# Optimization experiments

Measured on AMD Instinct MI355X. Metric: run time of the kernel, lower is better.

The kernel has to match this reference:

```python
import jax, jax.numpy as jnp
import numpy as np

HIDDEN = 1024
NUM_HEADS = 16
HEAD_DIM = HIDDEN // NUM_HEADS  # 64
ROPE_DIM = HEAD_DIM // 2        # 32 (per-axis rotary dim)
EPS = 1e-6


def _make_rope_tables(dim, grid_h, grid_w, theta=10000.0):
    # pt_seq_len == ft_seq_len, so t_h = arange(H), t_w = arange(W)
    freqs = 1.0 / theta ** (np.arange(0, dim, 2, dtype=np.float32)[: dim // 2] / dim)  # [dim//2]
    fh = np.repeat(np.outer(np.arange(grid_h, dtype=np.float32), freqs), 2, axis=-1)  # [H, dim]
    fw = np.repeat(np.outer(np.arange(grid_w, dtype=np.float32), freqs), 2, axis=-1)  # [W, dim]
    fh = np.broadcast_to(fh[:, None, :], (grid_h, grid_w, dim))
    fw = np.broadcast_to(fw[None, :, :], (grid_h, grid_w, dim))
    f2d = np.concatenate([fh, fw], axis=-1).reshape(grid_h * grid_w, 2 * dim)  # [HW, 2*dim]
    return jnp.asarray(np.cos(f2d)), jnp.asarray(np.sin(f2d))


def _rms_norm(x, w, eps=EPS):
    var = jnp.mean(jnp.square(x), axis=-1, keepdims=True)
    return x * jax.lax.rsqrt(var + eps) * w


def _rotate_half(x):
    x1 = x[..., 0::2]
    x2 = x[..., 1::2]
    return jnp.stack([-x2, x1], axis=-1).reshape(x.shape)


def _apply_rope(x, cos, sin):
    # x: [B, H, S, D]; cos/sin: [S, D]
    return x * cos + _rotate_half(x) * sin


def setup_inputs() -> dict:
    key = jax.random.key(0)
    ks = jax.random.split(key, 12)
    B, IMG_H, IMG_W, CND_H, CND_W = 2, 64, 64, 32, 32
    img_len, cnd_len = IMG_H * IMG_W, CND_H * CND_W
    xav = (6.0 / (HIDDEN + HIDDEN)) ** 0.5
    inp = {
        'image_tokens': jax.random.normal(ks[0], (B, img_len, HIDDEN), jnp.float32),
        'condition_tokens': jax.random.normal(ks[1], (B, cnd_len, HIDDEN), jnp.float32),
        'q_norm_w': jnp.ones((HIDDEN,), jnp.float32),
        'kv_norm_w': jnp.ones((HIDDEN,), jnp.float32),
        'q_head_norm_w': jnp.ones((HEAD_DIM,), jnp.float32),
        'k_head_norm_w': jnp.ones((HEAD_DIM,), jnp.float32),
        'q_w': jax.random.uniform(ks[2], (HIDDEN, HIDDEN), jnp.float32, -xav, xav),
        'q_b': jnp.zeros((HIDDEN,), jnp.float32),
        'k_w': jax.random.uniform(ks[3], (HIDDEN, HIDDEN), jnp.float32, -xav, xav),
        'k_b': jnp.zeros((HIDDEN,), jnp.float32),
        'v_w': jax.random.uniform(ks[4], (HIDDEN, HIDDEN), jnp.float32, -xav, xav),
        'v_b': jnp.zeros((HIDDEN,), jnp.float32),
        'o_w': jax.random.uniform(ks[5], (HIDDEN, HIDDEN), jnp.float32, -xav, xav),
        'o_b': jnp.zeros((HIDDEN,), jnp.float32),
        'alpha': jnp.full((1,), 0.5, jnp.float32),  # nonzero so backward exercises the attn path
    }
    ic, isn = _make_rope_tables(ROPE_DIM, IMG_H, IMG_W)
    cc, cs = _make_rope_tables(ROPE_DIM, CND_H, CND_W)
    inp.update(image_cos=ic, image_sin=isn, cond_cos=cc, cond_sin=cs)
    return inp


def reference(image_tokens, condition_tokens, q_norm_w, kv_norm_w, q_head_norm_w,
              k_head_norm_w, q_w, q_b, k_w, k_b, v_w, v_b, o_w, o_b, alpha,
              image_cos, image_sin, cond_cos, cond_sin):
    B, Li, _ = image_tokens.shape
    Lc = condition_tokens.shape[1]
    qn = _rms_norm(image_tokens, q_norm_w)
    kvn = _rms_norm(condition_tokens, kv_norm_w)
    # projections (torch Linear: x @ W.T + b); weights here stored [out, in]
    q = (qn @ q_w.T + q_b).reshape(B, Li, NUM_HEADS, HEAD_DIM).transpose(0, 2, 1, 3)
    k = (kvn @ k_w.T + k_b).reshape(B, Lc, NUM_HEADS, HEAD_DIM).transpose(0, 2, 1, 3)
    v = (kvn @ v_w.T + v_b).reshape(B, Lc, NUM_HEADS, HEAD_DIM).transpose(0, 2, 1, 3)
    q = _rms_norm(q, q_head_norm_w)
    k = _rms_norm(k, k_head_norm_w)
    q = _apply_rope(q, image_cos, image_sin)
    k = _apply_rope(k, cond_cos, cond_sin)
    scale = 1.0 / jnp.sqrt(jnp.asarray(HEAD_DIM, q.dtype))
    scores = jnp.einsum('bhqd,bhkd->bhqk', q, k) * scale
    attn = jax.nn.softmax(scores, axis=-1)
    out = jnp.einsum('bhqk,bhkd->bhqd', attn, v)
    out = out.transpose(0, 2, 1, 3).reshape(B, Li, HIDDEN)
    update = out @ o_w.T + o_b
    return image_tokens + alpha.reshape(1, 1, 1) * update
```

## Files before the change

### kernel.cpp

```cpp
#include <hip/hip_runtime.h>

typedef __bf16 bf16x8 __attribute__((ext_vector_type(8)));
typedef __bf16 bf16x4 __attribute__((ext_vector_type(4)));
typedef float  f32x4  __attribute__((ext_vector_type(4)));
typedef float  f32x16 __attribute__((ext_vector_type(16)));
typedef unsigned u32x2 __attribute__((ext_vector_type(2)));

#define DEVINL __device__ __forceinline__

DEVINL void gload_lds16(const void* g, void* l) {
  __builtin_amdgcn_global_load_lds((const __attribute__((address_space(1))) void*)g,
                                   (__attribute__((address_space(3))) void*)l, 16, 0, 0);
}

DEVINL unsigned pkbf(float a, float b) {
  union { __bf16 h[2]; unsigned u; } c;
  c.h[0] = (__bf16)a; c.h[1] = (__bf16)b;
  return c.u;
}

DEVINL float fast_exp2(float x) {
#if __has_builtin(__builtin_amdgcn_exp2f)
  return __builtin_amdgcn_exp2f(x);
#else
  float r;
  asm volatile("v_exp_f32 %0, %1" : "=v"(r) : "v"(x));
  return r;
#endif
}

DEVINL float2 swap32(float x) {
  u32x2 r = __builtin_amdgcn_permlane32_swap(__float_as_uint(x), __float_as_uint(x), false, false);
  return make_float2(__uint_as_float(r.x), __uint_as_float(r.y));
}

__global__ __launch_bounds__(256) void prep_kernel(
    const float* __restrict__ XA, const float* __restrict__ WA, __bf16* __restrict__ YA,
    const float* __restrict__ XB, const float* __restrict__ WB, __bf16* __restrict__ YB,
    const float* __restrict__ wq, const float* __restrict__ wk,
    const float* __restrict__ wv, const float* __restrict__ wo,
    __bf16* __restrict__ oq, __bf16* __restrict__ ok,
    __bf16* __restrict__ ov, __bf16* __restrict__ oo) {
  int rb = blockIdx.x, tid = threadIdx.x;
  if (rb < 10240) {
    const float* X; const float* W; __bf16* Y; int row;
    if (rb < 8192) { X = XA; W = WA; Y = YA; row = rb; }
    else { X = XB; W = WB; Y = YB; row = rb - 8192; }
    const float4* xr = (const float4*)(X + (size_t)row * 1024);
    float4 v = xr[tid];
    float ss = v.x * v.x + v.y * v.y + v.z * v.z + v.w * v.w;
#pragma unroll
    for (int m = 1; m < 64; m <<= 1) ss += __shfl_xor(ss, m);
    __shared__ float part[4];
    if ((tid & 63) == 0) part[tid >> 6] = ss;
    __syncthreads();
    float tot = part[0] + part[1] + part[2] + part[3];
    float rn = rsqrtf(tot * (1.0f / 1024.0f) + 1e-6f);
    float4 wv4 = ((const float4*)W)[tid];
    bf16x4 y;
    y[0] = (__bf16)(v.x * rn * wv4.x);
    y[1] = (__bf16)(v.y * rn * wv4.y);
    y[2] = (__bf16)(v.z * rn * wv4.z);
    y[3] = (__bf16)(v.w * rn * wv4.w);
    *(bf16x4*)(Y + (size_t)row * 1024 + tid * 4) = y;
  } else {
    int gid = (rb - 10240) * 256 + tid;
    int which = gid >> 17;
    size_t off = (size_t)(gid & 131071) * 8;
    const float* s = (which == 0) ? wq : (which == 1) ? wk : (which == 2) ? wv : wo;
    __bf16* o = (which == 0) ? oq : (which == 1) ? ok : (which == 2) ? ov : oo;
    float4 v0 = *(const float4*)(s + off), v1 = *(const float4*)(s + off + 4);
    bf16x8 y;
    y[0] = (__bf16)v0.x; y[1] = (__bf16)v0.y; y[2] = (__bf16)v0.z; y[3] = (__bf16)v0.w;
    y[4] = (__bf16)v1.x; y[5] = (__bf16)v1.y; y[6] = (__bf16)v1.z; y[7] = (__bf16)v1.w;
    *(bf16x8*)(o + off) = y;
  }
}

__global__ __launch_bounds__(256) void qkv_gemm_kernel(
    const __bf16* __restrict__ qn, const __bf16* __restrict__ kvn,
    const __bf16* __restrict__ wq, const __bf16* __restrict__ wkv,
    const float* __restrict__ qb, const float* __restrict__ kb, const float* __restrict__ vb,
    __bf16* __restrict__ Qt, __bf16* __restrict__ Kt, __bf16* __restrict__ Vt0) {
  __shared__ __attribute__((aligned(16))) __bf16 As[128 * 32];
  __shared__ __attribute__((aligned(16))) __bf16 Bs[128 * 32];
  int id = blockIdx.x;
  const __bf16 *A, *Bw; const float* bias; __bf16* Cout;
  int m0, n0, nloc;
  if (id < 512) {
    A = qn; Bw = wq; m0 = (id & 63) * 128; n0 = (id >> 6) * 128; nloc = n0;
    bias = qb; Cout = Qt;
  } else {
    int i2 = id - 512;
    A = kvn; Bw = wkv; m0 = (i2 & 15) * 128; n0 = (i2 >> 4) * 128;
    if (n0 < 1024) { bias = kb; Cout = Kt; nloc = n0; }
    else { bias = vb; Cout = Vt0; nloc = n0 - 1024; }
  }
  int tid = threadIdx.x, lane = tid & 63, w = tid >> 6, wr = w >> 1, wc = w & 1;
  f32x4 z4 = {0.f, 0.f, 0.f, 0.f};
  f32x4 acc[4][4];
#pragma unroll
  for (int i = 0; i < 4; i++)
#pragma unroll
    for (int j = 0; j < 4; j++) acc[i][j] = z4;

  for (int k0 = 0; k0 < 1024; k0 += 32) {
#pragma unroll
    for (int i = 0; i < 2; i++) {
      int chunk = i * 256 + tid;
      int row = chunk >> 2, cc = chunk & 3;
      gload_lds16(A + (size_t)(m0 + row) * 1024 + k0 + cc * 8, (char*)As + i * 4096 + w * 1024);
      gload_lds16(Bw + (size_t)(n0 + row) * 1024 + k0 + cc * 8, (char*)Bs + i * 4096 + w * 1024);
    }
    __syncthreads();
    bf16x8 af[4], bfr[4];
#pragma unroll
    for (int m = 0; m < 4; m++) {
      int r = wr * 64 + m * 16 + (lane & 15);
      af[m] = *(const bf16x8*)((const char*)As + r * 64 + ((lane >> 4) << 4));
    }
#pragma unroll
    for (int n = 0; n < 4; n++) {
      int r = wc * 64 + n * 16 + (lane & 15);
      bfr[n] = *(const bf16x8*)((const char*)Bs + r * 64 + ((lane >> 4) << 4));
    }
#pragma unroll
    for (int m = 0; m < 4; m++)
#pragma unroll
      for (int n = 0; n < 4; n++)
        acc[m][n] = __builtin_amdgcn_mfma_f32_16x16x32_bf16(af[m], bfr[n], acc[m][n], 0, 0, 0);
    __syncthreads();
  }

#pragma unroll
  for (int m = 0; m < 4; m++)
#pragma unroll
    for (int n = 0; n < 4; n++) {
      int col = nloc + wc * 64 + n * 16 + (lane & 15);
      float bv = bias[col];
#pragma unroll
      for (int r = 0; r < 4; r++) {
        int row = m0 + wr * 64 + m * 16 + ((lane >> 4) << 2) + r;
        size_t idx = ((size_t)row << 10) + col;
        Cout[idx] = (__bf16)(acc[m][n][r] + bv);
      }
    }
}

__global__ __launch_bounds__(256) void gemm_o_kernel(
    const __bf16* __restrict__ A, const __bf16* __restrict__ Bw,
    const float* __restrict__ bias, float* __restrict__ Cout,
    const float* __restrict__ resid, const float* __restrict__ alphap) {
  __shared__ __attribute__((aligned(16))) __bf16 As[128 * 32];
  __shared__ __attribute__((aligned(16))) __bf16 Bs[128 * 32];
  int tid = threadIdx.x, lane = tid & 63, w = tid >> 6, wr = w >> 1, wc = w & 1;
  int m0 = blockIdx.x * 128, n0 = blockIdx.y * 128;
  f32x4 z4 = {0.f, 0.f, 0.f, 0.f};
  f32x4 acc[4][4];
#pragma unroll
  for (int i = 0; i < 4; i++)
#pragma unroll
    for (int j = 0; j < 4; j++) acc[i][j] = z4;

  for (int k0 = 0; k0 < 1024; k0 += 32) {
#pragma unroll
    for (int i = 0; i < 2; i++) {
      int chunk = i * 256 + tid;
      int row = chunk >> 2, cc = chunk & 3;
      gload_lds16(A + (size_t)(m0 + row) * 1024 + k0 + cc * 8, (char*)As + i * 4096 + w * 1024);
      gload_lds16(Bw + (size_t)(n0 + row) * 1024 + k0 + cc * 8, (char*)Bs + i * 4096 + w * 1024);
    }
    __syncthreads();
    bf16x8 af[4], bfr[4];
#pragma unroll
    for (int m = 0; m < 4; m++) {
      int r = wr * 64 + m * 16 + (lane & 15);
      af[m] = *(const bf16x8*)((const char*)As + r * 64 + ((lane >> 4) << 4));
    }
#pragma unroll
    for (int n = 0; n < 4; n++) {
      int r = wc * 64 + n * 16 + (lane & 15);
      bfr[n] = *(const bf16x8*)((const char*)Bs + r * 64 + ((lane >> 4) << 4));
    }
#pragma unroll
    for (int m = 0; m < 4; m++)
#pragma unroll
      for (int n = 0; n < 4; n++)
        acc[m][n] = __builtin_amdgcn_mfma_f32_16x16x32_bf16(af[m], bfr[n], acc[m][n], 0, 0, 0);
    __syncthreads();
  }

  float aval = alphap[0];
#pragma unroll
  for (int m = 0; m < 4; m++)
#pragma unroll
    for (int n = 0; n < 4; n++) {
      int col = n0 + wc * 64 + n * 16 + (lane & 15);
      float bv = bias[col];
#pragma unroll
      for (int r = 0; r < 4; r++) {
        int row = m0 + wr * 64 + m * 16 + ((lane >> 4) << 2) + r;
        size_t idx = ((size_t)row << 10) + col;
        Cout[idx] = resid[idx] + aval * (acc[m][n][r] + bv);
      }
    }
}

__global__ __launch_bounds__(256) void kprep_kernel(
    const __bf16* __restrict__ Kt, const float* __restrict__ KHW,
    const float* __restrict__ CCOS, const float* __restrict__ CSIN,
    __bf16* __restrict__ Kr,
    const __bf16* __restrict__ V, __bf16* __restrict__ Vt) {
  int rb = blockIdx.x, tid = threadIdx.x;
  if (rb < 1024) {
    int inst = rb * 32 + (tid >> 3);
    int sub = tid & 7;
    int token = inst >> 4, h = inst & 15;
    int b = token >> 10, pos = token & 1023;
    const __bf16* xp = Kt + ((size_t)token << 10) + h * 64 + sub * 8;
    bf16x8 xv = *(const bf16x8*)xp;
    float xf[8];
#pragma unroll
    for (int i = 0; i < 8; i++) xf[i] = (float)xv[i];
    float ss = 0.f;
#pragma unroll
    for (int i = 0; i < 8; i++) ss += xf[i] * xf[i];
    ss += __shfl_xor(ss, 1);
    ss += __shfl_xor(ss, 2);
    ss += __shfl_xor(ss, 4);
    float rn = rsqrtf(ss * (1.0f / 64.0f) + 1e-6f);
    const float* hwp = KHW + sub * 8;
    const float* cp = CCOS + ((size_t)pos << 6) + sub * 8;
    const float* sp = CSIN + ((size_t)pos << 6) + sub * 8;
    float xn[8], o[8];
#pragma unroll
    for (int i = 0; i < 8; i++) xn[i] = xf[i] * rn * hwp[i];
#pragma unroll
    for (int i = 0; i < 8; i += 2) {
      o[i] = xn[i] * cp[i] - xn[i + 1] * sp[i];
      o[i + 1] = xn[i + 1] * cp[i + 1] + xn[i] * sp[i + 1];
    }
    bf16x8 yv;
#pragma unroll
    for (int i = 0; i < 8; i++) yv[i] = (__bf16)o[i];
    *(bf16x8*)(Kr + (((size_t)((b << 4) + h) << 10) + pos) * 64 + sub * 8) = yv;
  } else {
    int bx = rb - 1024;
    int bh = bx >> 4;
    int j0 = (bx & 15) * 64;
    int b = bh >> 4, h = bh & 15;
#pragma unroll
    for (int it = 0; it < 2; ++it) {
      int c = it * 256 + tid;
      int jl = c >> 3, d0 = (c & 7) * 8;
      bf16x8 v = *(const bf16x8*)(V + (size_t)(b * 1024 + j0 + jl) * 1024 + h * 64 + d0);
#pragma unroll
      for (int i = 0; i < 8; i++)
        Vt[((size_t)bh * 64 + d0 + i) * 1024 + j0 + jl] = v[i];
    }
  }
}

__global__ __launch_bounds__(256, 2) void attn_kernel(
    const __bf16* __restrict__ Qt, const float* __restrict__ QHW,
    const float* __restrict__ QCOS, const float* __restrict__ QSIN,
    const __bf16* __restrict__ Kr, const __bf16* __restrict__ Vtr,
    __bf16* __restrict__ AO) {
  int tid = threadIdx.x, lane = tid & 63, w = tid >> 6;
  int lq = lane & 31, hi = lane >> 5;
  int wgid = blockIdx.x;
  int nid = (wgid & 7) * 64 + (wgid >> 3);
  int q0 = (nid & 15) * 256;
  int bh = nid >> 4, b = bh >> 4, h = bh & 15;
  const float QSC = 0.125f * 1.44269504088896340736f;

  __shared__ __attribute__((aligned(16))) __bf16 Ks[3][4096];
  __shared__ __attribute__((aligned(16))) __bf16 Vs[3][4096];

  const __bf16* Kbh = Kr + ((size_t)bh << 16);
  const __bf16* Vbh = Vtr + ((size_t)bh << 16);

  auto STAGE = [&](int T, int BSEL) {
#pragma unroll
    for (int i = 0; i < 2; i++) {
      int s = 2 * w + i;
      int kt = s >> 2, ds2 = s & 3;
      gload_lds16(Kbh + (size_t)(T * 64 + kt * 32 + lq) * 64 + ds2 * 16 + hi * 8,
                  (char*)Ks[BSEL] + s * 1024);
      int f = s >> 1, dh = s & 1;
      gload_lds16(Vbh + (size_t)(dh * 32 + lq) * 1024 + T * 64 + f * 16 + hi * 8,
                  (char*)Vs[BSEL] + s * 1024);
    }
  };

  STAGE(0, 0);
  STAGE(1, 1);

  bf16x8 qf[2][4];
#pragma unroll
  for (int qt = 0; qt < 2; qt++) {
    int pos = q0 + w * 64 + qt * 32 + lq;
    const __bf16* qp = Qt + ((size_t)(b * 4096 + pos) << 10) + h * 64 + hi * 8;
    float xf[4][8];
    float ss = 0.f;
#pragma unroll
    for (int ds = 0; ds < 4; ds++) {
      bf16x8 xv = *(const bf16x8*)(qp + ds * 16);
#pragma unroll
      for (int j = 0; j < 8; j++) { float f = (float)xv[j]; xf[ds][j] = f; ss += f * f; }
    }
    float2 sw = swap32(ss);
    float rn = rsqrtf((sw.x + sw.y) * (1.0f / 64.0f) + 1e-6f);
#pragma unroll
    for (int ds = 0; ds < 4; ds++) {
      int d0 = ds * 16 + hi * 8;
      const float* wp = QHW + d0;
      const float* cp = QCOS + ((size_t)pos << 6) + d0;
      const float* sp = QSIN + ((size_t)pos << 6) + d0;
      float4 wa = *(const float4*)wp, wb = *(const float4*)(wp + 4);
      float4 ca = *(const float4*)cp, cb = *(const float4*)(cp + 4);
      float4 sa = *(const float4*)sp, sb = *(const float4*)(sp + 4);
      float wv[8] = {wa.x, wa.y, wa.z, wa.w, wb.x, wb.y, wb.z, wb.w};
      float cv[8] = {ca.x, ca.y, ca.z, ca.w, cb.x, cb.y, cb.z, cb.w};
      float sv[8] = {sa.x, sa.y, sa.z, sa.w, sb.x, sb.y, sb.z, sb.w};
      float xn[8];
#pragma unroll
      for (int j = 0; j < 8; j++) xn[j] = xf[ds][j] * rn * wv[j];
      bf16x8 q8;
#pragma unroll
      for (int j = 0; j < 8; j += 2) {
        q8[j]     = (__bf16)((xn[j] * cv[j] - xn[j + 1] * sv[j]) * QSC);
        q8[j + 1] = (__bf16)((xn[j + 1] * cv[j + 1] + xn[j] * sv[j + 1]) * QSC);
      }
      qf[qt][ds] = q8;
    }
  }

  f32x16 Z16;
#pragma unroll
  for (int r = 0; r < 16; r++) Z16[r] = 0.f;
  f32x16 accO[2][2];
#pragma unroll
  for (int qt = 0; qt < 2; qt++)
#pragma unroll
    for (int dh = 0; dh < 2; dh++) accO[qt][dh] = Z16;
  float srun[2] = {0.f, 0.f};

  asm volatile("s_waitcnt vmcnt(4)" ::: "memory");
  __builtin_amdgcn_s_barrier();
  asm volatile("" ::: "memory");

  int cur = 0, stg = 2;
  for (int t = 0; t < 16; t++) {
    if (t < 14) STAGE(t + 2, stg);
    const char* kbase = (const char*)Ks[cur];
    const char* vbase = (const char*)Vs[cur];
    int loff = lane * 16;

    bf16x8 kf[8], vf[8];
#pragma unroll
    for (int s = 0; s < 8; s++) kf[s] = *(const bf16x8*)(kbase + s * 1024 + loff);
#pragma unroll
    for (int s = 0; s < 8; s++) vf[s] = *(const bf16x8*)(vbase + s * 1024 + loff);

    f32x16 accS[2][2];
    __builtin_amdgcn_s_setprio(1);
#pragma unroll
    for (int qt = 0; qt < 2; qt++)
#pragma unroll
      for (int kt = 0; kt < 2; kt++) {
        accS[qt][kt] = __builtin_amdgcn_mfma_f32_32x32x16_bf16(kf[kt * 4], qf[qt][0], Z16, 0, 0, 0);
#pragma unroll
        for (int ds = 1; ds < 4; ds++)
          accS[qt][kt] = __builtin_amdgcn_mfma_f32_32x32x16_bf16(kf[kt * 4 + ds], qf[qt][ds], accS[qt][kt], 0, 0, 0);
      }
    __builtin_amdgcn_s_setprio(0);

    unsigned pa[2][4][4];
#pragma unroll
    for (int qt = 0; qt < 2; qt++) {
      float ssum = 0.f;
#pragma unroll
      for (int kt = 0; kt < 2; kt++)
#pragma unroll
        for (int r = 0; r < 16; r++) {
          float e = fast_exp2(accS[qt][kt][r]);
          accS[qt][kt][r] = e;
          ssum += e;
        }
      float2 sws = swap32(ssum);
      srun[qt] += sws.x + sws.y;
#pragma unroll
      for (int kt = 0; kt < 2; kt++)
#pragma unroll
        for (int s2 = 0; s2 < 2; s2++) {
          int f = kt * 2 + s2, rb = s2 * 8;
          unsigned u  = pkbf(accS[qt][kt][rb + 0], accS[qt][kt][rb + 1]);
          unsigned v2 = pkbf(accS[qt][kt][rb + 2], accS[qt][kt][rb + 3]);
          unsigned w2 = pkbf(accS[qt][kt][rb + 4], accS[qt][kt][rb + 5]);
          unsigned x2 = pkbf(accS[qt][kt][rb + 6], accS[qt][kt][rb + 7]);
          u32x2 r02 = __builtin_amdgcn_permlane32_swap(u, w2, false, false);
          u32x2 r13 = __builtin_amdgcn_permlane32_swap(v2, x2, false, false);
          pa[qt][f][0] = r02.x; pa[qt][f][1] = r13.x; pa[qt][f][2] = r02.y; pa[qt][f][3] = r13.y;
        }
    }

    __builtin_amdgcn_s_setprio(1);
#pragma unroll
    for (int f = 0; f < 4; f++)
#pragma unroll
      for (int qt = 0; qt < 2; qt++) {
        union { unsigned u[4]; bf16x8 v; } pf;
        pf.u[0] = pa[qt][f][0]; pf.u[1] = pa[qt][f][1];
        pf.u[2] = pa[qt][f][2]; pf.u[3] = pa[qt][f][3];
#pragma unroll
        for (int dh = 0; dh < 2; dh++)
          accO[qt][dh] = __builtin_amdgcn_mfma_f32_32x32x16_bf16(pf.v, vf[f * 2 + dh], accO[qt][dh], 0, 0, 0);
      }
    __builtin_amdgcn_s_setprio(0);

    if (t < 14) {
      asm volatile("s_waitcnt vmcnt(4)" ::: "memory");
      __builtin_amdgcn_s_barrier();
      asm volatile("" ::: "memory");
    } else if (t == 14) {
      asm volatile("s_waitcnt vmcnt(0)" ::: "memory");
      __builtin_amdgcn_s_barrier();
      asm volatile("" ::: "memory");
    }
    cur = (cur == 2) ? 0 : cur + 1;
    stg = (stg == 2) ? 0 : stg + 1;
  }

  __bf16* aobase = AO + (((size_t)b * 4096) << 10) + h * 64;
#pragma unroll
  for (int qt = 0; qt < 2; qt++) {
    float rinv = 1.0f / srun[qt];
    int ri = __float_as_int(rinv);
#pragma unroll
    for (int r = 0; r < 16; r++) {
      int cr = (r & 3) + ((r >> 2) << 3) + (hi << 2);
      float rv = __int_as_float(__builtin_amdgcn_ds_bpermute(cr << 2, ri));
      size_t rowoff = ((size_t)(q0 + w * 64 + qt * 32 + cr) << 10);
#pragma unroll
      for (int dh = 0; dh < 2; dh++)
        aobase[rowoff + dh * 32 + lq] = (__bf16)(accO[qt][dh][r] * rv);
    }
  }
}

extern "C" void kernel_launch(void* const* d_in, const int* in_sizes, int n_in,
                              void* d_out, int out_size, void* d_ws, size_t ws_size,
                              hipStream_t stream) {
  const float* img  = (const float*)d_in[0];
  const float* cnd  = (const float*)d_in[1];
  const float* qnw  = (const float*)d_in[2];
  const float* kvnw = (const float*)d_in[3];
  const float* qhw  = (const float*)d_in[4];
  const float* khw  = (const float*)d_in[5];
  const float* qw   = (const float*)d_in[6];
  const float* qb   = (const float*)d_in[7];
  const float* kw   = (const float*)d_in[8];
  const float* kb   = (const float*)d_in[9];
  const float* vw   = (const float*)d_in[10];
  const float* vb   = (const float*)d_in[11];
  const float* ow   = (const float*)d_in[12];
  const float* ob   = (const float*)d_in[13];
  const float* alpha= (const float*)d_in[14];
  const float* icos = (const float*)d_in[15];
  const float* isin = (const float*)d_in[16];
  const float* ccos = (const float*)d_in[17];
  const float* csin = (const float*)d_in[18];
  float* out = (float*)d_out;

  __bf16* p = (__bf16*)d_ws;
  __bf16* wqb = p; p += 1048576;
  __bf16* wkb = p; p += 1048576;
  __bf16* wvb = p; p += 1048576;
  __bf16* wob = p; p += 1048576;
  __bf16* qn  = p; p += 8388608;
  __bf16* kvn = p; p += 2097152;
  __bf16* Qt  = p; p += 8388608;
  __bf16* Kt  = p; p += 2097152;
  __bf16* Vt0 = p; p += 2097152;
  __bf16* Kr  = p; p += 2097152;
  __bf16* Vtr = p; p += 2097152;
  __bf16* AO  = qn;

  prep_kernel<<<12288, 256, 0, stream>>>(img, qnw, qn, cnd, kvnw, kvn,
                                         qw, kw, vw, ow, wqb, wkb, wvb, wob);

  qkv_gemm_kernel<<<768, 256, 0, stream>>>(qn, kvn, wqb, wkb, qb, kb, vb, Qt, Kt, Vt0);

  kprep_kernel<<<1536, 256, 0, stream>>>(Kt, khw, ccos, csin, Kr, Vt0, Vtr);

  attn_kernel<<<512, 256, 0, stream>>>(Qt, qhw, icos, isin, Kr, Vtr, AO);

  gemm_o_kernel<<<dim3(64, 8), 256, 0, stream>>>(AO, wob, ob, out, img, alpha);
}
```

Measured before the change: 158.0 us.

## Double-buffer GEMM K-loop and shrink attention tile to 128 queries per block

Factors the QKV and output GEMMs into a shared core that double-buffers LDS tiles, prefetching the next K-slice with async global-to-LDS loads while MFMAs run on the current one. This replaces the previous load-sync-compute-sync pattern. The attention kernel now handles 32 query rows per wave (128 per block) instead of 64, with a two-stage K/V buffer in place of three, twice as many blocks, and an occupancy hint of 3. Together these aim to hide memory latency and raise parallelism, at the cost of reloading each K/V tile twice as often and using more LDS in the GEMMs.

```diff
diff --git a/kernel.cpp b/kernel.cpp
--- a/kernel.cpp
+++ b/kernel.cpp
@@ -77,13 +77,74 @@
   }
 }
 
+template <typename EPIF>
+DEVINL void gemm_core(const __bf16* __restrict__ A, const __bf16* __restrict__ Bw,
+                      int m0, int n0, char* AsB, char* BsB, EPIF epi) {
+  int tid = threadIdx.x, lane = tid & 63, w = tid >> 6, wr = w >> 1, wc = w & 1;
+  f32x4 z4 = {0.f, 0.f, 0.f, 0.f};
+  f32x4 acc[4][4];
+#pragma unroll
+  for (int i = 0; i < 4; i++)
+#pragma unroll
+    for (int j = 0; j < 4; j++) acc[i][j] = z4;
+
+  auto STAGE = [&](int k0, int bsel) {
+#pragma unroll
+    for (int i = 0; i < 2; i++) {
+      int chunk = i * 256 + tid;
+      int row = chunk >> 2, cc = chunk & 3;
+      gload_lds16(A + (size_t)(m0 + row) * 1024 + k0 + cc * 8,
+                  AsB + bsel * 8192 + i * 4096 + w * 1024);
+      gload_lds16(Bw + (size_t)(n0 + row) * 1024 + k0 + cc * 8,
+                  BsB + bsel * 8192 + i * 4096 + w * 1024);
+    }
+  };
+
+  STAGE(0, 0);
+  int b = 0;
+  for (int it = 0; it < 32; ++it) {
+    if (it < 31) {
+      STAGE((it + 1) * 32, b ^ 1);
+      asm volatile("s_waitcnt vmcnt(4)" ::: "memory");
+    } else {
+      asm volatile("s_waitcnt vmcnt(0)" ::: "memory");
+    }
+    __builtin_amdgcn_s_barrier();
+    asm volatile("" ::: "memory");
+    const char* As = AsB + b * 8192;
+    const char* Bs = BsB + b * 8192;
+    bf16x8 af[4], bfr[4];
+#pragma unroll
+    for (int m = 0; m < 4; m++) {
+      int r = wr * 64 + m * 16 + (lane & 15);
+      af[m] = *(const bf16x8*)(As + r * 64 + ((lane >> 4) << 4));
+    }
+#pragma unroll
+    for (int n = 0; n < 4; n++) {
+      int r = wc * 64 + n * 16 + (lane & 15);
+      bfr[n] = *(const bf16x8*)(Bs + r * 64 + ((lane >> 4) << 4));
+    }
+    __builtin_amdgcn_s_setprio(1);
+#pragma unroll
+    for (int m = 0; m < 4; m++)
+#pragma unroll
+      for (int n = 0; n < 4; n++)
+        acc[m][n] = __builtin_amdgcn_mfma_f32_16x16x32_bf16(af[m], bfr[n], acc[m][n], 0, 0, 0);
+    __builtin_amdgcn_s_setprio(0);
+    __builtin_amdgcn_s_barrier();
+    asm volatile("" ::: "memory");
+    b ^= 1;
+  }
+  epi(acc, lane, wr, wc);
+}
+
 __global__ __launch_bounds__(256) void qkv_gemm_kernel(
     const __bf16* __restrict__ qn, const __bf16* __restrict__ kvn,
     const __bf16* __restrict__ wq, const __bf16* __restrict__ wkv,
     const float* __restrict__ qb, const float* __restrict__ kb, const float* __restrict__ vb,
     __bf16* __restrict__ Qt, __bf16* __restrict__ Kt, __bf16* __restrict__ Vt0) {
-  __shared__ __attribute__((aligned(16))) __bf16 As[128 * 32];
-  __shared__ __attribute__((aligned(16))) __bf16 Bs[128 * 32];
+  __shared__ __attribute__((aligned(16))) char AsB[2 * 8192];
+  __shared__ __attribute__((aligned(16))) char BsB[2 * 8192];
   int id = blockIdx.x;
   const __bf16 *A, *Bw; const float* bias; __bf16* Cout;
   int m0, n0, nloc;
@@ -96,114 +157,47 @@
     if (n0 < 1024) { bias = kb; Cout = Kt; nloc = n0; }
     else { bias = vb; Cout = Vt0; nloc = n0 - 1024; }
   }
-  int tid = threadIdx.x, lane = tid & 63, w = tid >> 6, wr = w >> 1, wc = w & 1;
-  f32x4 z4 = {0.f, 0.f, 0.f, 0.f};
-  f32x4 acc[4][4];
-#pragma unroll
-  for (int i = 0; i < 4; i++)
-#pragma unroll
-    for (int j = 0; j < 4; j++) acc[i][j] = z4;
-
-  for (int k0 = 0; k0 < 1024; k0 += 32) {
-#pragma unroll
-    for (int i = 0; i < 2; i++) {
-      int chunk = i * 256 + tid;
-      int row = chunk >> 2, cc = chunk & 3;
-      gload_lds16(A + (size_t)(m0 + row) * 1024 + k0 + cc * 8, (char*)As + i * 4096 + w * 1024);
-      gload_lds16(Bw + (size_t)(n0 + row) * 1024 + k0 + cc * 8, (char*)Bs + i * 4096 + w * 1024);
-    }
-    __syncthreads();
-    bf16x8 af[4], bfr[4];
-#pragma unroll
-    for (int m = 0; m < 4; m++) {
-      int r = wr * 64 + m * 16 + (lane & 15);
-      af[m] = *(const bf16x8*)((const char*)As + r * 64 + ((lane >> 4) << 4));
-    }
-#pragma unroll
-    for (int n = 0; n < 4; n++) {
-      int r = wc * 64 + n * 16 + (lane & 15);
-      bfr[n] = *(const bf16x8*)((const char*)Bs + r * 64 + ((lane >> 4) << 4));
-    }
-#pragma unroll
-    for (int m = 0; m < 4; m++)
-#pragma unroll
-      for (int n = 0; n < 4; n++)
-        acc[m][n] = __builtin_amdgcn_mfma_f32_16x16x32_bf16(af[m], bfr[n], acc[m][n], 0, 0, 0);
-    __syncthreads();
-  }
-
-#pragma unroll
-  for (int m = 0; m < 4; m++)
-#pragma unroll
-    for (int n = 0; n < 4; n++) {
-      int col = nloc + wc * 64 + n * 16 + (lane & 15);
-      float bv = bias[col];
-#pragma unroll
-      for (int r = 0; r < 4; r++) {
-        int row = m0 + wr * 64 + m * 16 + ((lane >> 4) << 2) + r;
-        size_t idx = ((size_t)row << 10) + col;
-        Cout[idx] = (__bf16)(acc[m][n][r] + bv);
-      }
-    }
+  gemm_core(A, Bw, m0, n0, AsB, BsB,
+            [&](f32x4 (&acc)[4][4], int lane, int wr, int wc) {
+#pragma unroll
+              for (int m = 0; m < 4; m++)
+#pragma unroll
+                for (int n = 0; n < 4; n++) {
+                  int col = nloc + wc * 64 + n * 16 + (lane & 15);
+                  float bv = bias[col];
+#pragma unroll
+                  for (int r = 0; r < 4; r++) {
+                    int row = m0 + wr * 64 + m * 16 + ((lane >> 4) << 2) + r;
+                    Cout[((size_t)row << 10) + col] = (__bf16)(acc[m][n][r] + bv);
+                  }
+                }
+            });
 }
 
 __global__ __launch_bounds__(256) void gemm_o_kernel(
     const __bf16* __restrict__ A, const __bf16* __restrict__ Bw,
     const float* __restrict__ bias, float* __restrict__ Cout,
     const float* __restrict__ resid, const float* __restrict__ alphap) {
-  __shared__ __attribute__((aligned(16))) __bf16 As[128 * 32];
-  __shared__ __attribute__((aligned(16))) __bf16 Bs[128 * 32];
-  int tid = threadIdx.x, lane = tid & 63, w = tid >> 6, wr = w >> 1, wc = w & 1;
+  __shared__ __attribute__((aligned(16))) char AsB[2 * 8192];
+  __shared__ __attribute__((aligned(16))) char BsB[2 * 8192];
   int m0 = blockIdx.x * 128, n0 = blockIdx.y * 128;
-  f32x4 z4 = {0.f, 0.f, 0.f, 0.f};
-  f32x4 acc[4][4];
-#pragma unroll
-  for (int i = 0; i < 4; i++)
-#pragma unroll
-    for (int j = 0; j < 4; j++) acc[i][j] = z4;
-
-  for (int k0 = 0; k0 < 1024; k0 += 32) {
-#pragma unroll
-    for (int i = 0; i < 2; i++) {
-      int chunk = i * 256 + tid;
-      int row = chunk >> 2, cc = chunk & 3;
-      gload_lds16(A + (size_t)(m0 + row) * 1024 + k0 + cc * 8, (char*)As + i * 4096 + w * 1024);
-      gload_lds16(Bw + (size_t)(n0 + row) * 1024 + k0 + cc * 8, (char*)Bs + i * 4096 + w * 1024);
-    }
-    __syncthreads();
-    bf16x8 af[4], bfr[4];
-#pragma unroll
-    for (int m = 0; m < 4; m++) {
-      int r = wr * 64 + m * 16 + (lane & 15);
-      af[m] = *(const bf16x8*)((const char*)As + r * 64 + ((lane >> 4) << 4));
-    }
-#pragma unroll
-    for (int n = 0; n < 4; n++) {
-      int r = wc * 64 + n * 16 + (lane & 15);
-      bfr[n] = *(const bf16x8*)((const char*)Bs + r * 64 + ((lane >> 4) << 4));
-    }
-#pragma unroll
-    for (int m = 0; m < 4; m++)
-#pragma unroll
-      for (int n = 0; n < 4; n++)
-        acc[m][n] = __builtin_amdgcn_mfma_f32_16x16x32_bf16(af[m], bfr[n], acc[m][n], 0, 0, 0);
-    __syncthreads();
-  }
-
   float aval = alphap[0];
-#pragma unroll
-  for (int m = 0; m < 4; m++)
-#pragma unroll
-    for (int n = 0; n < 4; n++) {
-      int col = n0 + wc * 64 + n * 16 + (lane & 15);
-      float bv = bias[col];
-#pragma unroll
-      for (int r = 0; r < 4; r++) {
-        int row = m0 + wr * 64 + m * 16 + ((lane >> 4) << 2) + r;
-        size_t idx = ((size_t)row << 10) + col;
-        Cout[idx] = resid[idx] + aval * (acc[m][n][r] + bv);
-      }
-    }
+  gemm_core(A, Bw, m0, n0, AsB, BsB,
+            [&](f32x4 (&acc)[4][4], int lane, int wr, int wc) {
+#pragma unroll
+              for (int m = 0; m < 4; m++)
+#pragma unroll
+                for (int n = 0; n < 4; n++) {
+                  int col = n0 + wc * 64 + n * 16 + (lane & 15);
+                  float bv = bias[col];
+#pragma unroll
+                  for (int r = 0; r < 4; r++) {
+                    int row = m0 + wr * 64 + m * 16 + ((lane >> 4) << 2) + r;
+                    size_t idx = ((size_t)row << 10) + col;
+                    Cout[idx] = resid[idx] + aval * (acc[m][n][r] + bv);
+                  }
+                }
+            });
 }
 
 __global__ __launch_bounds__(256) void kprep_kernel(
@@ -261,7 +255,7 @@
   }
 }
 
-__global__ __launch_bounds__(256, 2) void attn_kernel(
+__global__ __launch_bounds__(256, 3) void attn_kernel(
     const __bf16* __restrict__ Qt, const float* __restrict__ QHW,
     const float* __restrict__ QCOS, const float* __restrict__ QSIN,
     const __bf16* __restrict__ Kr, const __bf16* __restrict__ Vtr,
@@ -269,13 +263,13 @@
   int tid = threadIdx.x, lane = tid & 63, w = tid >> 6;
   int lq = lane & 31, hi = lane >> 5;
   int wgid = blockIdx.x;
-  int nid = (wgid & 7) * 64 + (wgid >> 3);
-  int q0 = (nid & 15) * 256;
-  int bh = nid >> 4, b = bh >> 4, h = bh & 15;
+  int nid = (wgid & 7) * 128 + (wgid >> 3);
+  int q0 = (nid & 31) * 128;
+  int bh = nid >> 5, b = bh >> 4, h = bh & 15;
   const float QSC = 0.125f * 1.44269504088896340736f;
 
-  __shared__ __attribute__((aligned(16))) __bf16 Ks[3][4096];
-  __shared__ __attribute__((aligned(16))) __bf16 Vs[3][4096];
+  __shared__ __attribute__((aligned(16))) __bf16 Ks[2][4096];
+  __shared__ __attribute__((aligned(16))) __bf16 Vs[2][4096];
 
   const __bf16* Kbh = Kr + ((size_t)bh << 16);
   const __bf16* Vbh = Vtr + ((size_t)bh << 16);
@@ -294,12 +288,10 @@
   };
 
   STAGE(0, 0);
-  STAGE(1, 1);
-
-  bf16x8 qf[2][4];
-#pragma unroll
-  for (int qt = 0; qt < 2; qt++) {
-    int pos = q0 + w * 64 + qt * 32 + lq;
+
+  bf16x8 qf[4];
+  {
+    int pos = q0 + w * 32 + lq;
     const __bf16* qp = Qt + ((size_t)(b * 4096 + pos) << 10) + h * 64 + hi * 8;
     float xf[4][8];
     float ss = 0.f;
@@ -332,120 +324,105 @@
         q8[j]     = (__bf16)((xn[j] * cv[j] - xn[j + 1] * sv[j]) * QSC);
         q8[j + 1] = (__bf16)((xn[j + 1] * cv[j + 1] + xn[j] * sv[j + 1]) * QSC);
       }
-      qf[qt][ds] = q8;
+      qf[ds] = q8;
     }
   }
 
   f32x16 Z16;
 #pragma unroll
   for (int r = 0; r < 16; r++) Z16[r] = 0.f;
-  f32x16 accO[2][2];
-#pragma unroll
-  for (int qt = 0; qt < 2; qt++)
-#pragma unroll
-    for (int dh = 0; dh < 2; dh++) accO[qt][dh] = Z16;
-  float srun[2] = {0.f, 0.f};
-
-  asm volatile("s_waitcnt vmcnt(4)" ::: "memory");
-  __builtin_amdgcn_s_barrier();
-  asm volatile("" ::: "memory");
-
-  int cur = 0, stg = 2;
+  f32x16 accO[2];
+  accO[0] = Z16; accO[1] = Z16;
+  float srun = 0.f;
+
+  int buf = 0;
   for (int t = 0; t < 16; t++) {
-    if (t < 14) STAGE(t + 2, stg);
-    const char* kbase = (const char*)Ks[cur];
-    const char* vbase = (const char*)Vs[cur];
+    if (t < 15) {
+      STAGE(t + 1, buf ^ 1);
+      asm volatile("s_waitcnt vmcnt(4)" ::: "memory");
+    } else {
+      asm volatile("s_waitcnt vmcnt(0)" ::: "memory");
+    }
+    __builtin_amdgcn_s_barrier();
+    asm volatile("" ::: "memory");
+
+    const char* kbase = (const char*)Ks[buf];
+    const char* vbase = (const char*)Vs[buf];
     int loff = lane * 16;
 
-    bf16x8 kf[8], vf[8];
+    bf16x8 kf[8];
 #pragma unroll
     for (int s = 0; s < 8; s++) kf[s] = *(const bf16x8*)(kbase + s * 1024 + loff);
+
+    f32x16 accS[2];
+    __builtin_amdgcn_s_setprio(1);
+#pragma unroll
+    for (int kt = 0; kt < 2; kt++) {
+      accS[kt] = __builtin_amdgcn_mfma_f32_32x32x16_bf16(kf[kt * 4], qf[0], Z16, 0, 0, 0);
+#pragma unroll
+      for (int ds = 1; ds < 4; ds++)
+        accS[kt] = __builtin_amdgcn_mfma_f32_32x32x16_bf16(kf[kt * 4 + ds], qf[ds], accS[kt], 0, 0, 0);
+    }
+    __builtin_amdgcn_s_setprio(0);
+
+    float ssum = 0.f;
+#pragma unroll
+    for (int kt = 0; kt < 2; kt++)
+#pragma unroll
+      for (int r = 0; r < 16; r++) {
+        float e = fast_exp2(accS[kt][r]);
+        accS[kt][r] = e;
+        ssum += e;
+      }
+    float2 sws = swap32(ssum);
+    srun += sws.x + sws.y;
+
+    unsigned pa[4][4];
+#pragma unroll
+    for (int kt = 0; kt < 2; kt++)
+#pragma unroll
+      for (int s2 = 0; s2 < 2; s2++) {
+        int f = kt * 2 + s2, rb = s2 * 8;
+        unsigned u  = pkbf(accS[kt][rb + 0], accS[kt][rb + 1]);
+        unsigned v2 = pkbf(accS[kt][rb + 2], accS[kt][rb + 3]);
+        unsigned w2 = pkbf(accS[kt][rb + 4], accS[kt][rb + 5]);
+        unsigned x2 = pkbf(accS[kt][rb + 6], accS[kt][rb + 7]);
+        u32x2 r02 = __builtin_amdgcn_permlane32_swap(u, w2, false, false);
+        u32x2 r13 = __builtin_amdgcn_permlane32_swap(v2, x2, false, false);
+        pa[f][0] = r02.x; pa[f][1] = r13.x; pa[f][2] = r02.y; pa[f][3] = r13.y;
+      }
+
+    bf16x8 vf[8];
 #pragma unroll
     for (int s = 0; s < 8; s++) vf[s] = *(const bf16x8*)(vbase + s * 1024 + loff);
 
-    f32x16 accS[2][2];
     __builtin_amdgcn_s_setprio(1);
 #pragma unroll
-    for (int qt = 0; qt < 2; qt++)
-#pragma unroll
-      for (int kt = 0; kt < 2; kt++) {
-        accS[qt][kt] = __builtin_amdgcn_mfma_f32_32x32x16_bf16(kf[kt * 4], qf[qt][0], Z16, 0, 0, 0);
-#pragma unroll
-        for (int ds = 1; ds < 4; ds++)
-          accS[qt][kt] = __builtin_amdgcn_mfma_f32_32x32x16_bf16(kf[kt * 4 + ds], qf[qt][ds], accS[qt][kt], 0, 0, 0);
-      }
+    for (int f = 0; f < 4; f++) {
+      union { unsigned u[4]; bf16x8 v; } pf;
+      pf.u[0] = pa[f][0]; pf.u[1] = pa[f][1]; pf.u[2] = pa[f][2]; pf.u[3] = pa[f][3];
+#pragma unroll
+      for (int dh = 0; dh < 2; dh++)
+        accO[dh] = __builtin_amdgcn_mfma_f32_32x32x16_bf16(pf.v, vf[f * 2 + dh], accO[dh], 0, 0, 0);
+    }
     __builtin_amdgcn_s_setprio(0);
 
-    unsigned pa[2][4][4];
-#pragma unroll
-    for (int qt = 0; qt < 2; qt++) {
-      float ssum = 0.f;
-#pragma unroll
-      for (int kt = 0; kt < 2; kt++)
-#pragma unroll
-        for (int r = 0; r < 16; r++) {
-          float e = fast_exp2(accS[qt][kt][r]);
-          accS[qt][kt][r] = e;
-          ssum += e;
-        }
-      float2 sws = swap32(ssum);
-      srun[qt] += sws.x + sws.y;
-#pragma unroll
-      for (int kt = 0; kt < 2; kt++)
-#pragma unroll
-        for (int s2 = 0; s2 < 2; s2++) {
-          int f = kt * 2 + s2, rb = s2 * 8;
-          unsigned u  = pkbf(accS[qt][kt][rb + 0], accS[qt][kt][rb + 1]);
-          unsigned v2 = pkbf(accS[qt][kt][rb + 2], accS[qt][kt][rb + 3]);
-          unsigned w2 = pkbf(accS[qt][kt][rb + 4], accS[qt][kt][rb + 5]);
-          unsigned x2 = pkbf(accS[qt][kt][rb + 6], accS[qt][kt][rb + 7]);
-          u32x2 r02 = __builtin_amdgcn_permlane32_swap(u, w2, false, false);
-          u32x2 r13 = __builtin_amdgcn_permlane32_swap(v2, x2, false, false);
-          pa[qt][f][0] = r02.x; pa[qt][f][1] = r13.x; pa[qt][f][2] = r02.y; pa[qt][f][3] = r13.y;
-        }
-    }
-
-    __builtin_amdgcn_s_setprio(1);
-#pragma unroll
-    for (int f = 0; f < 4; f++)
-#pragma unroll
-      for (int qt = 0; qt < 2; qt++) {
-        union { unsigned u[4]; bf16x8 v; } pf;
-        pf.u[0] = pa[qt][f][0]; pf.u[1] = pa[qt][f][1];
-        pf.u[2] = pa[qt][f][2]; pf.u[3] = pa[qt][f][3];
-#pragma unroll
-        for (int dh = 0; dh < 2; dh++)
-          accO[qt][dh] = __builtin_amdgcn_mfma_f32_32x32x16_bf16(pf.v, vf[f * 2 + dh], accO[qt][dh], 0, 0, 0);
-      }
-    __builtin_amdgcn_s_setprio(0);
-
-    if (t < 14) {
-      asm volatile("s_waitcnt vmcnt(4)" ::: "memory");
-      __builtin_amdgcn_s_barrier();
-      asm volatile("" ::: "memory");
-    } else if (t == 14) {
-      asm volatile("s_waitcnt vmcnt(0)" ::: "memory");
-      __builtin_amdgcn_s_barrier();
-      asm volatile("" ::: "memory");
-    }
-    cur = (cur == 2) ? 0 : cur + 1;
-    stg = (stg == 2) ? 0 : stg + 1;
+    __builtin_amdgcn_s_barrier();
+    asm volatile("" ::: "memory");
+    buf ^= 1;
   }
 
   __bf16* aobase = AO + (((size_t)b * 4096) << 10) + h * 64;
-#pragma unroll
-  for (int qt = 0; qt < 2; qt++) {
-    float rinv = 1.0f / srun[qt];
-    int ri = __float_as_int(rinv);
-#pragma unroll
-    for (int r = 0; r < 16; r++) {
-      int cr = (r & 3) + ((r >> 2) << 3) + (hi << 2);
-      float rv = __int_as_float(__builtin_amdgcn_ds_bpermute(cr << 2, ri));
-      size_t rowoff = ((size_t)(q0 + w * 64 + qt * 32 + cr) << 10);
-#pragma unroll
-      for (int dh = 0; dh < 2; dh++)
-        aobase[rowoff + dh * 32 + lq] = (__bf16)(accO[qt][dh][r] * rv);
-    }
+  float rinv = 1.0f / srun;
+  int ri = __float_as_int(rinv);
+#pragma unroll
+  for (int r = 0; r < 16; r++) {
+    int cr = (r & 3) + ((r >> 2) << 3) + (hi << 2);
+    float rv = __int_as_float(__builtin_amdgcn_ds_bpermute(cr << 2, ri));
+    size_t rowoff = ((size_t)(q0 + w * 32 + cr) << 10);
+#pragma unroll
+    for (int dh = 0; dh < 2; dh++)
+      aobase[rowoff + dh * 32 + lq] = (__bf16)(accO[dh][r] * rv);
   }
 }
 
@@ -494,7 +471,7 @@
 
   kprep_kernel<<<1536, 256, 0, stream>>>(Kt, khw, ccos, csin, Kr, Vt0, Vtr);
 
-  attn_kernel<<<512, 256, 0, stream>>>(Qt, qhw, icos, isin, Kr, Vtr, AO);
+  attn_kernel<<<1024, 256, 0, stream>>>(Qt, qhw, icos, isin, Kr, Vtr, AO);
 
   gemm_o_kernel<<<dim3(64, 8), 256, 0, stream>>>(AO, wob, ob, out, img, alpha);
 }
```

New measurement: 152.0 us. 3.8% less time.
